# Optimization experiments

Measured on AMD Instinct MI355X. Metric: run time of the kernel, lower is better.

The kernel has to match this reference:

```python
import jax, jax.numpy as jnp
import numpy as np

N_NODES = 100000
N_EDGES = 640000
DIM = 128
N_LAYERS = 3

def setup_inputs() -> dict:
    key = jax.random.key(0)
    k1, k2, k3 = jax.random.split(key, 3)
    x = jax.random.normal(k1, (1, N_NODES, DIM), dtype=jnp.float32)
    edge_index = jax.random.randint(k2, (2, N_EDGES), 0, N_NODES, dtype=jnp.int64)
    Ws = jax.random.normal(k3, (N_LAYERS, DIM, DIM), dtype=jnp.float32) * (1.0 / np.sqrt(DIM))
    bs = jnp.zeros((N_LAYERS, DIM), dtype=jnp.float32)
    return {"x": x, "edge_index": edge_index, "Ws": Ws, "bs": bs}

def reference(x, edge_index, Ws, bs):
    # Stacked PyG-style GCNConv layers with ReLU, as in GraphEncoder (gnn_type='gcn').
    # GCNConv: add self-loops, symmetric norm D^-1/2 A D^-1/2, h W, scatter-sum, + bias.
    h = x[0]                                  # [N, D] (squeeze batch dim of 1)
    N = h.shape[0]
    loops = jnp.arange(N, dtype=edge_index.dtype)
    src = jnp.concatenate([edge_index[0], loops])   # [E+N] message sources
    dst = jnp.concatenate([edge_index[1], loops])   # [E+N] aggregation targets
    deg = jax.ops.segment_sum(jnp.ones_like(dst, dtype=h.dtype), dst, num_segments=N)
    dinv = jnp.where(deg > 0, jax.lax.rsqrt(deg), 0.0)
    norm = (dinv[src] * dinv[dst])[:, None]         # [E+N, 1] edge weights
    for l in range(Ws.shape[0]):
        m = norm * (h @ Ws[l])[src]                 # gather + per-edge message
        h = jax.ops.segment_sum(m, dst, num_segments=N) + bs[l]
        h = jax.nn.relu(h)
    return h[None]                                  # [1, N, D]
```

## Files before the change

### kernel.cpp

```cpp
#include <hip/hip_runtime.h>

#define DIM 128
#define MROW 272

typedef unsigned int uint32;
typedef short bf16x8 __attribute__((ext_vector_type(8)));
typedef float f32x4 __attribute__((ext_vector_type(4)));

__device__ __forceinline__ unsigned short f2b(float f) {
    return (unsigned short)((__float_as_uint(f) + 0x8000u) >> 16);
}
__device__ __forceinline__ uint32 packbf2(float lo, float hi) {
    uint32 a = __float_as_uint(lo);
    uint32 b = __float_as_uint(hi);
    return ((a + 0x8000u) >> 16) | ((b + 0x8000u) & 0xffff0000u);
}
__device__ __forceinline__ float bflo(uint32 u) { return __uint_as_float(u << 16); }
__device__ __forceinline__ float bfhi(uint32 u) { return __uint_as_float(u & 0xffff0000u); }

__global__ __launch_bounds__(256) void k_count(const int* __restrict__ dst,
                                               int* __restrict__ cnt, int E) {
    int e = blockIdx.x * 256 + threadIdx.x;
    if (e < E) atomicAdd(&cnt[dst[e]], 1);
}

__global__ __launch_bounds__(256) void k_scaleg(const float* __restrict__ x,
                                                const float* __restrict__ dinv,
                                                uint32* __restrict__ g, int n) {
    int t = blockIdx.x * 256 + threadIdx.x;
    if (t >= n * 64) return;
    int node = t >> 6;
    float dv = dinv[node];
    float2 v = ((const float2*)x)[t];
    g[t] = packbf2(dv * v.x, dv * v.y);
}

__global__ __launch_bounds__(256) void k_scan1(const int* __restrict__ cnt,
                                               int* __restrict__ incl,
                                               int* __restrict__ bsums,
                                               float* __restrict__ dinv, int n) {
    __shared__ int tmp[256];
    int i = blockIdx.x * 256 + threadIdx.x;
    int t = threadIdx.x;
    int c = (i < n) ? cnt[i] : 0;
    if (i < n) dinv[i] = rsqrtf((float)(c + 1));
    tmp[t] = c;
    __syncthreads();
#pragma unroll
    for (int off = 1; off < 256; off <<= 1) {
        int v = (t >= off) ? tmp[t - off] : 0;
        __syncthreads();
        tmp[t] += v;
        __syncthreads();
    }
    if (i < n) incl[i] = tmp[t];
    if (t == 255) bsums[blockIdx.x] = tmp[255];
}

__global__ __launch_bounds__(512) void k_scan2(int* __restrict__ bsums, int nb) {
    __shared__ int tmp[512];
    int t = threadIdx.x;
    tmp[t] = (t < nb) ? bsums[t] : 0;
    __syncthreads();
#pragma unroll
    for (int off = 1; off < 512; off <<= 1) {
        int v = (t >= off) ? tmp[t - off] : 0;
        __syncthreads();
        tmp[t] += v;
        __syncthreads();
    }
    if (t < nb) bsums[t] = (t == 0) ? 0 : tmp[t - 1];
}

__global__ __launch_bounds__(256) void k_scan3(int* __restrict__ incl,
                                               const int* __restrict__ bsums, int n) {
    int i = blockIdx.x * 256 + threadIdx.x;
    if (i < n) incl[i] += bsums[blockIdx.x];
}

__global__ __launch_bounds__(256) void k_fill(const int* __restrict__ src,
                                              const int* __restrict__ dst,
                                              int* __restrict__ incl,
                                              int* __restrict__ srcs, int E) {
    int e = blockIdx.x * 256 + threadIdx.x;
    if (e >= E) return;
    int p = atomicSub(&incl[dst[e]], 1) - 1;
    srcs[p] = src[e];
}

__global__ __launch_bounds__(256) void k_prepW(const float* __restrict__ Ws,
                                               short* __restrict__ Wb, int total) {
    int t = blockIdx.x * 256 + threadIdx.x;
    if (t >= total) return;
    int layer = t >> 14;
    int idx = t & 16383;
    int j = idx & 7;
    int l = (idx >> 3) & 63;
    int f = idx >> 9;
    int ks = f & 3;
    int cs = (f >> 2) & 1;
    int w = f >> 3;
    int nn = w * 32 + cs * 16 + (l & 15);
    int kk = ks * 32 + (l >> 4) * 8 + j;
    Wb[t] = (short)f2b(Ws[(size_t)layer * DIM * DIM + kk * DIM + nn]);
}

__global__ __launch_bounds__(256) void k_layer(const uint32* __restrict__ g,
                                               const int* __restrict__ srcs,
                                               const int* __restrict__ rowptr,
                                               const float* __restrict__ dinv,
                                               const short* __restrict__ Wb,
                                               const float* __restrict__ bias,
                                               uint32* __restrict__ Gn,
                                               float* __restrict__ Out,
                                               int n, int E, int final_layer) {
    __shared__ __align__(16) char smem[32 * MROW];
    __shared__ int rowS[33];
    int tid = threadIdx.x;
    int w = tid >> 6;
    int lane = tid & 63;
    int row0 = blockIdx.x * 32;

    if (tid < 33) {
        int r = row0 + tid;
        rowS[tid] = (r < n) ? rowptr[r] : E;
    }
    __syncthreads();

    {
        int hw = tid >> 5;
        int sub = tid & 31;
        const uint2* g2 = (const uint2*)g;
#pragma unroll
        for (int i = 0; i < 2; ++i) {
            int nlA = hw * 4 + 2 * i;
            int nlB = nlA + 1;
            int nodeA = row0 + nlA;
            int nodeB = row0 + nlB;
            int pA = rowS[nlA], qA = rowS[nlA + 1];
            int pB = rowS[nlB], qB = rowS[nlB + 1];
            float dA = (nodeA < n) ? dinv[nodeA] : 0.f;
            float dB = (nodeB < n) ? dinv[nodeB] : 0.f;
            uint2 z = make_uint2(0u, 0u);
            uint2 uA = (nodeA < n) ? g2[(size_t)nodeA * 32 + sub] : z;
            uint2 uB = (nodeB < n) ? g2[(size_t)nodeB * 32 + sub] : z;
            float aA0 = bflo(uA.x), aA1 = bfhi(uA.x), aA2 = bflo(uA.y), aA3 = bfhi(uA.y);
            float aB0 = bflo(uB.x), aB1 = bfhi(uB.x), aB2 = bflo(uB.y), aB3 = bfhi(uB.y);
            int nb = max(qA - pA, qB - pB);
            for (int t = 0; t < nb; t += 4) {
                int sA[4], sB[4];
                float mA[4], mB[4];
#pragma unroll
                for (int u = 0; u < 4; ++u) {
                    int eA = pA + t + u;
                    int eB = pB + t + u;
                    mA[u] = (eA < qA) ? 1.f : 0.f;
                    mB[u] = (eB < qB) ? 1.f : 0.f;
                    int iA = max(min(eA, qA - 1), pA);
                    int iB = max(min(eB, qB - 1), pB);
                    sA[u] = srcs[iA];
                    sB[u] = srcs[iB];
                }
                uint2 vA[4], vB[4];
#pragma unroll
                for (int u = 0; u < 4; ++u) {
                    vA[u] = g2[(size_t)sA[u] * 32 + sub];
                    vB[u] = g2[(size_t)sB[u] * 32 + sub];
                }
#pragma unroll
                for (int u = 0; u < 4; ++u) {
                    aA0 = fmaf(mA[u], bflo(vA[u].x), aA0);
                    aA1 = fmaf(mA[u], bfhi(vA[u].x), aA1);
                    aA2 = fmaf(mA[u], bflo(vA[u].y), aA2);
                    aA3 = fmaf(mA[u], bfhi(vA[u].y), aA3);
                    aB0 = fmaf(mB[u], bflo(vB[u].x), aB0);
                    aB1 = fmaf(mB[u], bfhi(vB[u].x), aB1);
                    aB2 = fmaf(mB[u], bflo(vB[u].y), aB2);
                    aB3 = fmaf(mB[u], bfhi(vB[u].y), aB3);
                }
            }
            uint2 oA, oB;
            oA.x = packbf2(dA * aA0, dA * aA1);
            oA.y = packbf2(dA * aA2, dA * aA3);
            oB.x = packbf2(dB * aB0, dB * aB1);
            oB.y = packbf2(dB * aB2, dB * aB3);
            *(uint2*)(smem + nlA * MROW + sub * 8) = oA;
            *(uint2*)(smem + nlB * MROW + sub * 8) = oB;
        }
    }
    __syncthreads();
    __builtin_amdgcn_sched_barrier(0);

    const bf16x8* wb = (const bf16x8*)Wb;
    bf16x8 bfrag[2][4];
#pragma unroll
    for (int cs = 0; cs < 2; ++cs)
#pragma unroll
        for (int ks = 0; ks < 4; ++ks)
            bfrag[cs][ks] = wb[((w * 2 + cs) * 4 + ks) * 64 + lane];

    int lr = lane & 15;
    int lg = lane >> 4;

    f32x4 acc[2][2];
#pragma unroll
    for (int rs = 0; rs < 2; ++rs)
#pragma unroll
        for (int cs = 0; cs < 2; ++cs) acc[rs][cs] = (f32x4){0.f, 0.f, 0.f, 0.f};

    const char* base0 = smem + lr * MROW + lg * 16;
    const char* base1 = smem + (16 + lr) * MROW + lg * 16;
#pragma unroll
    for (int ks = 0; ks < 4; ++ks) {
        bf16x8 a0 = *(const bf16x8*)(base0 + ks * 64);
        bf16x8 a1 = *(const bf16x8*)(base1 + ks * 64);
#pragma unroll
        for (int cs = 0; cs < 2; ++cs) {
            acc[0][cs] = __builtin_amdgcn_mfma_f32_16x16x32_bf16(a0, bfrag[cs][ks], acc[0][cs], 0, 0, 0);
            acc[1][cs] = __builtin_amdgcn_mfma_f32_16x16x32_bf16(a1, bfrag[cs][ks], acc[1][cs], 0, 0, 0);
        }
    }

    float b0 = bias[w * 32 + lr];
    float b1 = bias[w * 32 + 16 + lr];

#pragma unroll
    for (int rs = 0; rs < 2; ++rs)
#pragma unroll
        for (int r = 0; r < 4; ++r) {
            int grow = row0 + rs * 16 + lg * 4 + r;
            if (grow < n) {
                float h0 = fmaxf(acc[rs][0][r] + b0, 0.f);
                float h1 = fmaxf(acc[rs][1][r] + b1, 0.f);
                if (final_layer) {
                    Out[(size_t)grow * DIM + w * 32 + lr]      = h0;
                    Out[(size_t)grow * DIM + w * 32 + 16 + lr] = h1;
                } else {
                    float dv = dinv[grow];
                    unsigned short* gp = (unsigned short*)Gn;
                    gp[(size_t)grow * DIM + w * 32 + lr]      = f2b(dv * h0);
                    gp[(size_t)grow * DIM + w * 32 + 16 + lr] = f2b(dv * h1);
                }
            }
        }
}

extern "C" void kernel_launch(void* const* d_in, const int* in_sizes, int n_in,
                              void* d_out, int out_size, void* d_ws, size_t ws_size,
                              hipStream_t stream) {
    const float* x  = (const float*)d_in[0];
    const int*   ei = (const int*)d_in[1];
    const float* Ws = (const float*)d_in[2];
    const float* bs = (const float*)d_in[3];

    const int N = in_sizes[0] / DIM;
    const int E = in_sizes[1] / 2;
    const int L = in_sizes[2] / (DIM * DIM);

    const int* src = ei;
    const int* dst = ei + E;

    float* out = (float*)d_out;

    char* ws = (char*)d_ws;
    uint32* g0   = (uint32*)ws;                ws += (size_t)N * 64 * 4;
    uint32* g1   = (uint32*)ws;                ws += (size_t)N * 64 * 4;
    short* Wb    = (short*)ws;                 ws += (size_t)L * 16384 * 2;
    float* dinv  = (float*)ws;                 ws += (size_t)N * 4;
    int*   cnt   = (int*)ws;                   ws += (size_t)N * 4;
    int*   incl  = (int*)ws;                   ws += (size_t)N * 4;
    int*   srcs  = (int*)ws;                   ws += (size_t)E * 4;
    int*   bsums = (int*)ws;                   ws += 512 * 4;

    const int nbN = (N + 255) / 256;
    const int nbE = (E + 255) / 256;
    const int totW = L * 16384;

    k_prepW<<<(totW + 255) / 256, 256, 0, stream>>>(Ws, Wb, totW);
    hipMemsetAsync(cnt, 0, (size_t)N * 4, stream);
    k_count<<<nbE, 256, 0, stream>>>(dst, cnt, E);
    k_scan1<<<nbN, 256, 0, stream>>>(cnt, incl, bsums, dinv, N);
    k_scan2<<<1, 512, 0, stream>>>(bsums, nbN);
    k_scaleg<<<(N * 64 + 255) / 256, 256, 0, stream>>>(x, dinv, g0, N);
    k_scan3<<<nbN, 256, 0, stream>>>(incl, bsums, N);
    k_fill <<<nbE, 256, 0, stream>>>(src, dst, incl, srcs, E);

    const int nblk = (N + 31) / 32;
    uint32* gin = g0;
    for (int l = 0; l < L; ++l) {
        uint32* gout = (gin == g0) ? g1 : g0;
        k_layer<<<nblk, 256, 0, stream>>>(gin, srcs, incl, dinv,
                                          Wb + (size_t)l * 16384,
                                          bs + (size_t)l * DIM,
                                          gout, out, N, E, l == L - 1);
        gin = gout;
    }
}
```

Before: 309.4 us.

## Stage edge sources in LDS and gather via zero sentinel row with deeper unroll

Each half-wave preloads the source indices for its four nodes into shared memory, so the gather loop reads indices from LDS and no longer issues dependent global loads. Padded edges point at a zero sentinel row (node n), which is appended to both feature buffers and to dinv, so the per-edge mask multiply becomes a plain add. The gather unroll goes from 4 to 8 edges per node pair to keep more loads in flight. The cost is 8 KB of extra LDS per block, which may reduce occupancy, plus a global-index fallback path for node groups with too many edges.

```diff
diff --git a/kernel.cpp b/kernel.cpp
--- a/kernel.cpp
+++ b/kernel.cpp
@@ -2,6 +2,7 @@
 
 #define DIM 128
 #define MROW 272
+#define ECAP 256
 
 typedef unsigned int uint32;
 typedef short bf16x8 __attribute__((ext_vector_type(8)));
@@ -25,9 +26,15 @@
 }
 
 __global__ __launch_bounds__(256) void k_scaleg(const float* __restrict__ x,
-                                                const float* __restrict__ dinv,
-                                                uint32* __restrict__ g, int n) {
+                                                float* __restrict__ dinv,
+                                                uint32* __restrict__ g,
+                                                uint32* __restrict__ g1, int n) {
     int t = blockIdx.x * 256 + threadIdx.x;
+    if (blockIdx.x == 0 && threadIdx.x < 64) {
+        g [(size_t)n * 64 + threadIdx.x] = 0u;
+        g1[(size_t)n * 64 + threadIdx.x] = 0u;
+        if (threadIdx.x == 0) dinv[n] = 0.f;
+    }
     if (t >= n * 64) return;
     int node = t >> 6;
     float dv = dinv[node];
@@ -115,6 +122,7 @@
                                                float* __restrict__ Out,
                                                int n, int E, int final_layer) {
     __shared__ __align__(16) char smem[32 * MROW];
+    __shared__ int eL[8][ECAP];
     __shared__ int rowS[33];
     int tid = threadIdx.x;
     int w = tid >> 6;
@@ -130,55 +138,65 @@
     {
         int hw = tid >> 5;
         int sub = tid & 31;
-        const uint2* g2 = (const uint2*)g;
+        int base4 = hw * 4;
+        int p0 = rowS[base4];
+        int cnt = rowS[base4 + 4] - p0;
+        bool useL = (cnt <= ECAP - 8);
+        if (useL) {
+            for (int j = sub; j < cnt; j += 32) eL[hw][j] = srcs[p0 + j];
+            if (sub < 8) eL[hw][cnt + sub] = n;
+        }
+
+        const char* gB = (const char*)g;
+        uint32 subOff = (uint32)(sub << 3);
+        int Em1 = E - 1;
+
 #pragma unroll
         for (int i = 0; i < 2; ++i) {
-            int nlA = hw * 4 + 2 * i;
+            int nlA = base4 + 2 * i;
             int nlB = nlA + 1;
-            int nodeA = row0 + nlA;
-            int nodeB = row0 + nlB;
-            int pA = rowS[nlA], qA = rowS[nlA + 1];
-            int pB = rowS[nlB], qB = rowS[nlB + 1];
-            float dA = (nodeA < n) ? dinv[nodeA] : 0.f;
-            float dB = (nodeB < n) ? dinv[nodeB] : 0.f;
-            uint2 z = make_uint2(0u, 0u);
-            uint2 uA = (nodeA < n) ? g2[(size_t)nodeA * 32 + sub] : z;
-            uint2 uB = (nodeB < n) ? g2[(size_t)nodeB * 32 + sub] : z;
+            int pA = rowS[nlA] - p0, qA = rowS[nlA + 1] - p0;
+            int pB = qA,              qB = rowS[nlB + 1] - p0;
+            int nodeA = min(row0 + nlA, n);
+            int nodeB = min(row0 + nlB, n);
+            float dA = dinv[nodeA];
+            float dB = dinv[nodeB];
+            uint2 uA = *(const uint2*)(gB + (((uint32)nodeA) << 8) + subOff);
+            uint2 uB = *(const uint2*)(gB + (((uint32)nodeB) << 8) + subOff);
             float aA0 = bflo(uA.x), aA1 = bfhi(uA.x), aA2 = bflo(uA.y), aA3 = bfhi(uA.y);
             float aB0 = bflo(uB.x), aB1 = bfhi(uB.x), aB2 = bflo(uB.y), aB3 = bfhi(uB.y);
             int nb = max(qA - pA, qB - pB);
-            for (int t = 0; t < nb; t += 4) {
-                int sA[4], sB[4];
-                float mA[4], mB[4];
-#pragma unroll
-                for (int u = 0; u < 4; ++u) {
-                    int eA = pA + t + u;
-                    int eB = pB + t + u;
-                    mA[u] = (eA < qA) ? 1.f : 0.f;
-                    mB[u] = (eB < qB) ? 1.f : 0.f;
-                    int iA = max(min(eA, qA - 1), pA);
-                    int iB = max(min(eB, qB - 1), pB);
-                    sA[u] = srcs[iA];
-                    sB[u] = srcs[iB];
-                }
-                uint2 vA[4], vB[4];
-#pragma unroll
-                for (int u = 0; u < 4; ++u) {
-                    vA[u] = g2[(size_t)sA[u] * 32 + sub];
-                    vB[u] = g2[(size_t)sB[u] * 32 + sub];
-                }
-#pragma unroll
-                for (int u = 0; u < 4; ++u) {
-                    aA0 = fmaf(mA[u], bflo(vA[u].x), aA0);
-                    aA1 = fmaf(mA[u], bfhi(vA[u].x), aA1);
-                    aA2 = fmaf(mA[u], bflo(vA[u].y), aA2);
-                    aA3 = fmaf(mA[u], bfhi(vA[u].y), aA3);
-                    aB0 = fmaf(mB[u], bflo(vB[u].x), aB0);
-                    aB1 = fmaf(mB[u], bfhi(vB[u].x), aB1);
-                    aB2 = fmaf(mB[u], bflo(vB[u].y), aB2);
-                    aB3 = fmaf(mB[u], bfhi(vB[u].y), aB3);
-                }
+
+#define GLOOP(FETCH)                                                      \
+            for (int t = 0; t < nb; t += 8) {                             \
+                uint2 vA[8], vB[8];                                       \
+                _Pragma("unroll")                                         \
+                for (int u = 0; u < 8; ++u) {                             \
+                    int eA = pA + t + u;                                  \
+                    int eB = pB + t + u;                                  \
+                    int iA = FETCH(eA);                                   \
+                    int iB = FETCH(eB);                                   \
+                    iA = (eA < qA) ? iA : n;                              \
+                    iB = (eB < qB) ? iB : n;                              \
+                    vA[u] = *(const uint2*)(gB + (((uint32)iA) << 8) + subOff); \
+                    vB[u] = *(const uint2*)(gB + (((uint32)iB) << 8) + subOff); \
+                }                                                         \
+                _Pragma("unroll")                                         \
+                for (int u = 0; u < 8; ++u) {                             \
+                    aA0 += bflo(vA[u].x); aA1 += bfhi(vA[u].x);           \
+                    aA2 += bflo(vA[u].y); aA3 += bfhi(vA[u].y);           \
+                    aB0 += bflo(vB[u].x); aB1 += bfhi(vB[u].x);           \
+                    aB2 += bflo(vB[u].y); aB3 += bfhi(vB[u].y);           \
+                }                                                         \
             }
+
+#define FETCH_LDS(e) (eL[hw][(e)])
+#define FETCH_GLB(e) (srcs[min(p0 + (e), Em1)])
+            if (useL) { GLOOP(FETCH_LDS) } else { GLOOP(FETCH_GLB) }
+#undef FETCH_LDS
+#undef FETCH_GLB
+#undef GLOOP
+
             uint2 oA, oB;
             oA.x = packbf2(dA * aA0, dA * aA1);
             oA.y = packbf2(dA * aA2, dA * aA3);
@@ -263,10 +281,10 @@
     float* out = (float*)d_out;
 
     char* ws = (char*)d_ws;
-    uint32* g0   = (uint32*)ws;                ws += (size_t)N * 64 * 4;
-    uint32* g1   = (uint32*)ws;                ws += (size_t)N * 64 * 4;
+    uint32* g0   = (uint32*)ws;                ws += (size_t)(N + 1) * 64 * 4;
+    uint32* g1   = (uint32*)ws;                ws += (size_t)(N + 1) * 64 * 4;
     short* Wb    = (short*)ws;                 ws += (size_t)L * 16384 * 2;
-    float* dinv  = (float*)ws;                 ws += (size_t)N * 4;
+    float* dinv  = (float*)ws;                 ws += (size_t)(N + 1) * 4;
     int*   cnt   = (int*)ws;                   ws += (size_t)N * 4;
     int*   incl  = (int*)ws;                   ws += (size_t)N * 4;
     int*   srcs  = (int*)ws;                   ws += (size_t)E * 4;
@@ -281,7 +299,7 @@
     k_count<<<nbE, 256, 0, stream>>>(dst, cnt, E);
     k_scan1<<<nbN, 256, 0, stream>>>(cnt, incl, bsums, dinv, N);
     k_scan2<<<1, 512, 0, stream>>>(bsums, nbN);
-    k_scaleg<<<(N * 64 + 255) / 256, 256, 0, stream>>>(x, dinv, g0, N);
+    k_scaleg<<<(N * 64 + 255) / 256, 256, 0, stream>>>(x, dinv, g0, g1, N);
     k_scan3<<<nbN, 256, 0, stream>>>(incl, bsums, N);
     k_fill <<<nbE, 256, 0, stream>>>(src, dst, incl, srcs, E);
 
```

Result: no change. 315.5 us (+2.0%).
